# Kernel tuning notes

Hardware: AMD Instinct MI355X
Metric: run time of the kernel (lower is better)

The kernel has to match this reference:

```python
import jax, jax.numpy as jnp
import numpy as np

BUCKETS = 1 << 22          # hash table size (power of two)
RES = 1.0 / 1024.0         # voxel resolution
D = 8                      # features per voxel
N_PTS = 2_000_000
# 8 trilinear corner offsets, same order as _corner_offsets()
CORNER_OFFSETS = np.array([[0, 0, 0], [1, 0, 0], [0, 1, 0], [1, 1, 0],
                           [0, 0, 1], [1, 0, 1], [0, 1, 1], [1, 1, 1]], dtype=np.uint32)


def setup_inputs() -> dict:
    key = jax.random.key(0)
    k1, k2 = jax.random.split(key)
    pts = jax.random.uniform(k1, (N_PTS, 3), dtype=jnp.float32)           # in [0,1)
    voxel_features = jax.random.normal(k2, (BUCKETS, D), dtype=jnp.float32) * 0.01
    primes = jnp.array([1, 2654435761, 805459861], dtype=jnp.uint32)
    return {"pts": pts, "voxel_features": voxel_features, "primes": primes}


def reference(pts, voxel_features, primes):
    # --- _grid_indices (hash mode, one_to_one=False) ---
    q = pts / RES                                   # (N,3) continuous grid coords
    base = jnp.floor(q).astype(jnp.int32)           # (N,3), non-negative by construction
    offs = jnp.asarray(CORNER_OFFSETS)              # (8,3) uint32
    idx = base[:, None, :].astype(jnp.uint32) + offs[None, :, :]  # (N,8,3)

    # --- _lookup: spatial hash. uint32 wraparound == torch int64 sum mod 2^32,
    # and since BUCKETS divides 2^32, % BUCKETS matches torch exactly. ---
    vid = (idx * primes[None, None, :]).sum(-1) % jnp.uint32(BUCKETS)  # (N,8)
    feat = voxel_features[vid]                      # (N,8,D) hashed gather

    # --- trilinear weights ---
    frac = q - base.astype(q.dtype)                 # (N,3)
    wx = jnp.stack([1.0 - frac[:, 0], frac[:, 0]], axis=1)
    wy = jnp.stack([1.0 - frac[:, 1], frac[:, 1]], axis=1)
    wz = jnp.stack([1.0 - frac[:, 2], frac[:, 2]], axis=1)
    w = (wx[:, [0, 1, 0, 1, 0, 1, 0, 1]]
         * wy[:, [0, 0, 1, 1, 0, 0, 1, 1]]
         * wz[:, [0, 0, 0, 0, 1, 1, 1, 1]])         # (N,8)
    return (feat * w[..., None]).sum(axis=1)        # (N,D)
```

## Files before the change

kernel.cpp:

```cpp
#include <hip/hip_runtime.h>

#define BUCKETS_LOG2 22
#define BUCKET_MASK ((1u << BUCKETS_LOG2) - 1u)
#define BLOCK 256

typedef float f32x4 __attribute__((ext_vector_type(4)));

__global__ __launch_bounds__(BLOCK) void hash_trilerp_kernel(
    const float* __restrict__ pts,
    const float* __restrict__ vf,
    const unsigned int* __restrict__ primes,
    float* __restrict__ out,
    int n)
{
    __shared__ float sp[3 * BLOCK];

    const int tid = threadIdx.x;
    const int i = blockIdx.x * BLOCK + tid;

    {
        const int base = blockIdx.x * BLOCK * 3;
        const int total = n * 3;
        #pragma unroll
        for (int k = 0; k < 3; ++k) {
            int idx = base + k * BLOCK + tid;
            if (idx < total) sp[k * BLOCK + tid] = pts[idx];
        }
    }
    __syncthreads();

    if (i >= n) return;

    const unsigned int p0 = primes[0];
    const unsigned int p1 = primes[1];
    const unsigned int p2 = primes[2];

    const float px = sp[3 * tid + 0];
    const float py = sp[3 * tid + 1];
    const float pz = sp[3 * tid + 2];

    const float qx = px * 1024.0f;
    const float qy = py * 1024.0f;
    const float qz = pz * 1024.0f;

    const float bxf = floorf(qx);
    const float byf = floorf(qy);
    const float bzf = floorf(qz);
    const float fx = qx - bxf, fy = qy - byf, fz = qz - bzf;

    const unsigned int bx = (unsigned int)(int)bxf;
    const unsigned int by = (unsigned int)(int)byf;
    const unsigned int bz = (unsigned int)(int)bzf;

    unsigned int hx[2], hy[2], hz[2];
    hx[0] = bx * p0; hx[1] = hx[0] + p0;
    hy[0] = by * p1; hy[1] = hy[0] + p1;
    hz[0] = bz * p2; hz[1] = hz[0] + p2;

    unsigned int boff[8];
    #pragma unroll
    for (int c = 0; c < 8; ++c) {
        const int cx = c & 1, cy = (c >> 1) & 1, cz = (c >> 2) & 1;
        const unsigned int vid = (hx[cx] + hy[cy] + hz[cz]) & BUCKET_MASK;
        boff[c] = vid << 5;
    }

    f32x4 f0, f1, f2, f3, f4, f5, f6, f7, f8, f9, f10, f11, f12, f13, f14, f15;
    #define GLD(dst, off, imm) \
        asm volatile("global_load_dwordx4 %0, %1, %2 offset:" #imm \
                     : "=v"(dst) : "v"(off), "s"(vf))
    GLD(f0,  boff[0], 0);  GLD(f1,  boff[0], 16);
    GLD(f2,  boff[1], 0);  GLD(f3,  boff[1], 16);
    GLD(f4,  boff[2], 0);  GLD(f5,  boff[2], 16);
    GLD(f6,  boff[3], 0);  GLD(f7,  boff[3], 16);
    GLD(f8,  boff[4], 0);  GLD(f9,  boff[4], 16);
    GLD(f10, boff[5], 0);  GLD(f11, boff[5], 16);
    GLD(f12, boff[6], 0);  GLD(f13, boff[6], 16);
    GLD(f14, boff[7], 0);  GLD(f15, boff[7], 16);
    #undef GLD

    asm volatile("s_waitcnt vmcnt(0)"
                 : "+v"(f0), "+v"(f1), "+v"(f2), "+v"(f3),
                   "+v"(f4), "+v"(f5), "+v"(f6), "+v"(f7),
                   "+v"(f8), "+v"(f9), "+v"(f10), "+v"(f11),
                   "+v"(f12), "+v"(f13), "+v"(f14), "+v"(f15)
                 :: "memory");

    const float wx[2] = { 1.0f - fx, fx };
    const float wy[2] = { 1.0f - fy, fy };
    const float wz[2] = { 1.0f - fz, fz };

    float w[8];
    #pragma unroll
    for (int c = 0; c < 8; ++c) {
        const int cx = c & 1, cy = (c >> 1) & 1, cz = (c >> 2) & 1;
        w[c] = wx[cx] * wy[cy] * wz[cz];
    }

    f32x4 a0 = { 0.f, 0.f, 0.f, 0.f };
    f32x4 a1 = { 0.f, 0.f, 0.f, 0.f };
    a0 += w[0] * f0;  a1 += w[0] * f1;
    a0 += w[1] * f2;  a1 += w[1] * f3;
    a0 += w[2] * f4;  a1 += w[2] * f5;
    a0 += w[3] * f6;  a1 += w[3] * f7;
    a0 += w[4] * f8;  a1 += w[4] * f9;
    a0 += w[5] * f10; a1 += w[5] * f11;
    a0 += w[6] * f12; a1 += w[6] * f13;
    a0 += w[7] * f14; a1 += w[7] * f15;

    f32x4* __restrict__ o4 = (f32x4*)out;
    __builtin_nontemporal_store(a0, &o4[(size_t)i * 2u]);
    __builtin_nontemporal_store(a1, &o4[(size_t)i * 2u + 1u]);
}

extern "C" void kernel_launch(void* const* d_in, const int* in_sizes, int n_in,
                              void* d_out, int out_size, void* d_ws, size_t ws_size,
                              hipStream_t stream) {
    const float* pts            = (const float*)d_in[0];
    const float* vf             = (const float*)d_in[1];
    const unsigned int* primes  = (const unsigned int*)d_in[2];
    float* out                  = (float*)d_out;

    const int n = in_sizes[0] / 3;
    const int grid = (n + BLOCK - 1) / BLOCK;
    hash_trilerp_kernel<<<grid, BLOCK, 0, stream>>>(pts, vf, primes, out, n);
}
```

Before: 369.9 us.

## Split each point across two threads, one per half of the feature row

```diff
diff --git a/kernel.cpp b/kernel.cpp
--- a/kernel.cpp
+++ b/kernel.cpp
@@ -3,6 +3,7 @@
 #define BUCKETS_LOG2 22
 #define BUCKET_MASK ((1u << BUCKETS_LOG2) - 1u)
 #define BLOCK 256
+#define PTS_PER_BLOCK (BLOCK / 2)
 
 typedef float f32x4 __attribute__((ext_vector_type(4)));
 
@@ -13,31 +14,34 @@
     float* __restrict__ out,
     int n)
 {
-    __shared__ float sp[3 * BLOCK];
+    __shared__ float sp[3 * PTS_PER_BLOCK];
 
     const int tid = threadIdx.x;
-    const int i = blockIdx.x * BLOCK + tid;
+    const int pbase = blockIdx.x * PTS_PER_BLOCK;
 
     {
-        const int base = blockIdx.x * BLOCK * 3;
         const int total = n * 3;
+        const int gbase = pbase * 3;
         #pragma unroll
-        for (int k = 0; k < 3; ++k) {
-            int idx = base + k * BLOCK + tid;
-            if (idx < total) sp[k * BLOCK + tid] = pts[idx];
+        for (int j = tid; j < 3 * PTS_PER_BLOCK; j += BLOCK) {
+            const int g = gbase + j;
+            if (g < total) sp[j] = pts[g];
         }
     }
     __syncthreads();
 
-    if (i >= n) return;
+    const int lp = tid >> 1;
+    const int p  = pbase + lp;
+    const unsigned int h = (unsigned int)(tid & 1);
+    if (p >= n) return;
 
     const unsigned int p0 = primes[0];
     const unsigned int p1 = primes[1];
     const unsigned int p2 = primes[2];
 
-    const float px = sp[3 * tid + 0];
-    const float py = sp[3 * tid + 1];
-    const float pz = sp[3 * tid + 2];
+    const float px = sp[3 * lp + 0];
+    const float py = sp[3 * lp + 1];
+    const float pz = sp[3 * lp + 2];
 
     const float qx = px * 1024.0f;
     const float qy = py * 1024.0f;
@@ -57,34 +61,28 @@
     hy[0] = by * p1; hy[1] = hy[0] + p1;
     hz[0] = bz * p2; hz[1] = hz[0] + p2;
 
+    const unsigned int hoff = h << 4;
     unsigned int boff[8];
     #pragma unroll
     for (int c = 0; c < 8; ++c) {
         const int cx = c & 1, cy = (c >> 1) & 1, cz = (c >> 2) & 1;
         const unsigned int vid = (hx[cx] + hy[cy] + hz[cz]) & BUCKET_MASK;
-        boff[c] = vid << 5;
+        boff[c] = (vid << 5) | hoff;
     }
 
-    f32x4 f0, f1, f2, f3, f4, f5, f6, f7, f8, f9, f10, f11, f12, f13, f14, f15;
-    #define GLD(dst, off, imm) \
-        asm volatile("global_load_dwordx4 %0, %1, %2 offset:" #imm \
+    f32x4 f0, f1, f2, f3, f4, f5, f6, f7;
+    #define GLD(dst, off) \
+        asm volatile("global_load_dwordx4 %0, %1, %2" \
                      : "=v"(dst) : "v"(off), "s"(vf))
-    GLD(f0,  boff[0], 0);  GLD(f1,  boff[0], 16);
-    GLD(f2,  boff[1], 0);  GLD(f3,  boff[1], 16);
-    GLD(f4,  boff[2], 0);  GLD(f5,  boff[2], 16);
-    GLD(f6,  boff[3], 0);  GLD(f7,  boff[3], 16);
-    GLD(f8,  boff[4], 0);  GLD(f9,  boff[4], 16);
-    GLD(f10, boff[5], 0);  GLD(f11, boff[5], 16);
-    GLD(f12, boff[6], 0);  GLD(f13, boff[6], 16);
-    GLD(f14, boff[7], 0);  GLD(f15, boff[7], 16);
+    GLD(f0, boff[0]);
+    GLD(f1, boff[1]);
+    GLD(f2, boff[2]);
+    GLD(f3, boff[3]);
+    GLD(f4, boff[4]);
+    GLD(f5, boff[5]);
+    GLD(f6, boff[6]);
+    GLD(f7, boff[7]);
     #undef GLD
-
-    asm volatile("s_waitcnt vmcnt(0)"
-                 : "+v"(f0), "+v"(f1), "+v"(f2), "+v"(f3),
-                   "+v"(f4), "+v"(f5), "+v"(f6), "+v"(f7),
-                   "+v"(f8), "+v"(f9), "+v"(f10), "+v"(f11),
-                   "+v"(f12), "+v"(f13), "+v"(f14), "+v"(f15)
-                 :: "memory");
 
     const float wx[2] = { 1.0f - fx, fx };
     const float wy[2] = { 1.0f - fy, fy };
@@ -97,20 +95,23 @@
         w[c] = wx[cx] * wy[cy] * wz[cz];
     }
 
-    f32x4 a0 = { 0.f, 0.f, 0.f, 0.f };
-    f32x4 a1 = { 0.f, 0.f, 0.f, 0.f };
-    a0 += w[0] * f0;  a1 += w[0] * f1;
-    a0 += w[1] * f2;  a1 += w[1] * f3;
-    a0 += w[2] * f4;  a1 += w[2] * f5;
-    a0 += w[3] * f6;  a1 += w[3] * f7;
-    a0 += w[4] * f8;  a1 += w[4] * f9;
-    a0 += w[5] * f10; a1 += w[5] * f11;
-    a0 += w[6] * f12; a1 += w[6] * f13;
-    a0 += w[7] * f14; a1 += w[7] * f15;
+    asm volatile("s_waitcnt vmcnt(0)"
+                 : "+v"(f0), "+v"(f1), "+v"(f2), "+v"(f3),
+                   "+v"(f4), "+v"(f5), "+v"(f6), "+v"(f7)
+                 :: "memory");
+
+    f32x4 a = { 0.f, 0.f, 0.f, 0.f };
+    a += w[0] * f0;
+    a += w[1] * f1;
+    a += w[2] * f2;
+    a += w[3] * f3;
+    a += w[4] * f4;
+    a += w[5] * f5;
+    a += w[6] * f6;
+    a += w[7] * f7;
 
     f32x4* __restrict__ o4 = (f32x4*)out;
-    __builtin_nontemporal_store(a0, &o4[(size_t)i * 2u]);
-    __builtin_nontemporal_store(a1, &o4[(size_t)i * 2u + 1u]);
+    __builtin_nontemporal_store(a, &o4[(size_t)p * 2u + h]);
 }
 
 extern "C" void kernel_launch(void* const* d_in, const int* in_sizes, int n_in,
@@ -122,6 +123,6 @@
     float* out                  = (float*)d_out;
 
     const int n = in_sizes[0] / 3;
-    const int grid = (n + BLOCK - 1) / BLOCK;
+    const int grid = (n + PTS_PER_BLOCK - 1) / PTS_PER_BLOCK;
     hash_trilerp_kernel<<<grid, BLOCK, 0, stream>>>(pts, vf, primes, out, n);
 }
```

Measured after the change: 362.9 us. Within noise of the previous version (-1.9%).
